# Performance work log

Hardware: AMD Instinct MI355X
Metric: run time of the kernel (lower is better)

## Reference

```python
import jax, jax.numpy as jnp
import numpy as np

N, E = 100000, 1000000
IN_DIM, OUT_DIM, HEADS = 64, 64, 4
C = OUT_DIM // HEADS  # per-head channels = 16
NEG_SLOPE = 0.2
SOFTMAX_EPS = 1e-16  # PyG softmax denominator epsilon
LN_EPS = 1e-5


def setup_inputs() -> dict:
    key = jax.random.key(0)
    ks = jax.random.split(key, 8)
    node_input = jax.random.normal(ks[0], (N, IN_DIM), dtype=jnp.float32)
    edge_index = jax.random.randint(ks[1], (2, E), 0, N, dtype=jnp.int64)
    # GATConv params (glorot-ish scale)
    W = jax.random.normal(ks[2], (IN_DIM, HEADS * C), dtype=jnp.float32) / np.sqrt(IN_DIM)
    att_src = jax.random.normal(ks[3], (HEADS, C), dtype=jnp.float32) / np.sqrt(C)
    att_dst = jax.random.normal(ks[4], (HEADS, C), dtype=jnp.float32) / np.sqrt(C)
    bias = jnp.zeros((HEADS * C,), dtype=jnp.float32)
    # LayerNorm params
    gamma = jnp.ones((OUT_DIM,), dtype=jnp.float32)
    beta = jnp.zeros((OUT_DIM,), dtype=jnp.float32)
    return {"node_input": node_input, "edge_index": edge_index, "W": W,
            "att_src": att_src, "att_dst": att_dst, "bias": bias,
            "gamma": gamma, "beta": beta}


def _gat_forward(x, edge_index, W, att_src, att_dst, bias, gamma, beta):
    src, dst = edge_index[0], edge_index[1]  # message flows src -> dst
    h = (x @ W).reshape(N, HEADS, C)                       # [N, H, C]
    a_src = jnp.einsum('nhc,hc->nh', h, att_src)           # [N, H]
    a_dst = jnp.einsum('nhc,hc->nh', h, att_dst)           # [N, H]
    # per-edge attention logits + leaky relu
    e = a_src[src] + a_dst[dst]                            # [E, H]
    e = jnp.where(e >= 0, e, NEG_SLOPE * e)
    # segment softmax over incoming edges of each target node
    m = jax.ops.segment_max(e, dst, num_segments=N)        # [N, H]
    m = jnp.where(jnp.isfinite(m), m, 0.0)                 # empty segments -> 0
    ex = jnp.exp(e - m[dst])                               # [E, H]
    denom = jax.ops.segment_sum(ex, dst, num_segments=N)   # [N, H]
    alpha = ex / (denom[dst] + SOFTMAX_EPS)                # [E, H]
    # weighted scatter-sum of source features
    msg = alpha[:, :, None] * h[src]                       # [E, H, C]
    out = jax.ops.segment_sum(msg, dst, num_segments=N)    # [N, H, C]
    out = out.reshape(N, HEADS * C) + bias                 # concat heads + bias
    # LayerNorm
    mu = out.mean(axis=-1, keepdims=True)
    var = out.var(axis=-1, keepdims=True)
    out = (out - mu) * jax.lax.rsqrt(var + LN_EPS) * gamma + beta
    # query gate is dead code (graph is a dict -> hasattr fails); dropout is eval identity
    return out


def reference(node_input, edge_index, W, att_src, att_dst, bias, gamma, beta):
    return _gat_forward(node_input, edge_index, W, att_src, att_dst, bias, gamma, beta)
```

## Files before the change

### kernel.cpp

```cpp
#include <hip/hip_runtime.h>
#include <hip/hip_bf16.h>
#include <math.h>

#define N_NODES 100000
#define E_EDGES 1000000
#define HEADS 4
#define DIM 64
#define NEG_SLOPE 0.2f
#define SM_EPS 1e-16f
#define LN_EPS 1e-5f
#define P1_BLOCKS 256
#define NT16 6250
#define GEMM_BLOCKS 1563
#define FEAT_BLOCKS (P1_BLOCKS + GEMM_BLOCKS)
#define CHUNK 3907
#define EPT 16
#define BUCKET_W 512
#define NBUCK 196

typedef __attribute__((ext_vector_type(8))) short short8v;
typedef __attribute__((ext_vector_type(4))) float f32x4;

static __device__ __forceinline__ unsigned short bfh(float f) {
    __hip_bfloat16 b = __float2bfloat16(f);
    return *reinterpret_cast<unsigned short*>(&b);
}
static __device__ __forceinline__ float bfh2f(unsigned short u) {
    return __uint_as_float((unsigned)u << 16);
}

__global__ __launch_bounds__(256) void k_wprep(
        const float* __restrict__ W, uint4* __restrict__ Wf) {
    int t = threadIdx.x;
    for (int e = t; e < 1024; e += 256) {
        int l = e & 63, f = e >> 6;
        int s = f & 1, kh = (f >> 1) & 1, n = f >> 2;
        int c = n * 16 + (l & 15);
        int k0 = kh * 32 + (l >> 4) * 8;
        unsigned short hw[8];
#pragma unroll
        for (int j = 0; j < 8; ++j) {
            float wv = W[(k0 + j) * 64 + c];
            unsigned short hi = bfh(wv);
            hw[j] = s ? bfh(wv - bfh2f(hi)) : hi;
        }
        uint4 pk;
        pk.x = hw[0] | ((unsigned)hw[1] << 16);
        pk.y = hw[2] | ((unsigned)hw[3] << 16);
        pk.z = hw[4] | ((unsigned)hw[5] << 16);
        pk.w = hw[6] | ((unsigned)hw[7] << 16);
        Wf[e] = pk;
    }
}

__global__ __launch_bounds__(256) void k_feat(
        const float* __restrict__ x, const float* __restrict__ Wf_,
        const float* __restrict__ att_src, const float* __restrict__ att_dst,
        const int* __restrict__ ei, __hip_bfloat16* __restrict__ hb,
        float* __restrict__ asrc, float* __restrict__ adst,
        int2* __restrict__ chunkbuf, int* __restrict__ pre) {
    __shared__ __align__(16) int smem_i[8326];
    int t = threadIdx.x;

    if (blockIdx.x < P1_BLOCKS) {
        int2* out2 = (int2*)smem_i;
        int*  cnt  = smem_i + 2 * CHUNK;
        int*  scan = cnt + 256;
        int base_e = blockIdx.x * CHUNK;
        int es[EPT], ed[EPT];
#pragma unroll
        for (int k = 0; k < EPT; ++k) {
            int i = k * 256 + t;
            int e = base_e + i;
            bool v = (i < CHUNK) && (e < E_EDGES);
            es[k] = v ? ei[e] : 0;
            ed[k] = v ? ei[E_EDGES + e] : -1;
        }
        cnt[t] = 0;
        __syncthreads();
#pragma unroll
        for (int k = 0; k < EPT; ++k)
            if (ed[k] >= 0) atomicAdd(&cnt[ed[k] >> 9], 1);
        __syncthreads();
        scan[t] = (t < NBUCK) ? cnt[t] : 0;
        __syncthreads();
#pragma unroll
        for (int off = 1; off < 256; off <<= 1) {
            int v = (t >= off) ? scan[t - off] : 0;
            __syncthreads();
            scan[t] += v;
            __syncthreads();
        }
        int excl = (t == 0) ? 0 : scan[t - 1];
        if (t < NBUCK) pre[blockIdx.x * (NBUCK + 1) + t] = excl;
        if (t == 0)    pre[blockIdx.x * (NBUCK + 1) + NBUCK] = scan[NBUCK - 1];
        if (t < NBUCK) cnt[t] = excl;
        __syncthreads();
#pragma unroll
        for (int k = 0; k < EPT; ++k)
            if (ed[k] >= 0) {
                int pos = atomicAdd(&cnt[ed[k] >> 9], 1);
                out2[pos] = make_int2(es[k], ed[k]);
            }
        __syncthreads();
        int ec = E_EDGES - base_e; ec = (ec > CHUNK) ? CHUNK : ec;
        for (int i = t; i < ec; i += 256)
            chunkbuf[base_e + i] = out2[i];
        return;
    }

    int w = t >> 6, lane = t & 63;
    int tile = (blockIdx.x - P1_BLOCKS) * 4 + w;
    if (tile >= NT16) return;
    int base = tile * 16;
    int m = lane & 15, kg = lane >> 4;

    const float* xr = x + (size_t)(base + m) * 64 + kg * 8;
    short8v ah[2], al[2];
#pragma unroll
    for (int kh = 0; kh < 2; ++kh) {
        float4 q0 = *(const float4*)(xr + kh * 32);
        float4 q1 = *(const float4*)(xr + kh * 32 + 4);
        float qq[8] = {q0.x, q0.y, q0.z, q0.w, q1.x, q1.y, q1.z, q1.w};
#pragma unroll
        for (int j = 0; j < 8; ++j) {
            unsigned short h = bfh(qq[j]);
            ah[kh][j] = (short)h;
            al[kh][j] = (short)bfh(qq[j] - bfh2f(h));
        }
    }

    const short8v* Wfv = (const short8v*)Wf_;
    float vs_keep = 0.f, vd_keep = 0.f;
#pragma unroll
    for (int n = 0; n < 4; ++n) {
        short8v bh0 = Wfv[((n * 2 + 0) * 2 + 0) * 64 + lane];
        short8v bl0 = Wfv[((n * 2 + 0) * 2 + 1) * 64 + lane];
        short8v bh1 = Wfv[((n * 2 + 1) * 2 + 0) * 64 + lane];
        short8v bl1 = Wfv[((n * 2 + 1) * 2 + 1) * 64 + lane];
        f32x4 a4 = {0.f, 0.f, 0.f, 0.f};
        a4 = __builtin_amdgcn_mfma_f32_16x16x32_bf16(ah[0], bh0, a4, 0, 0, 0);
        a4 = __builtin_amdgcn_mfma_f32_16x16x32_bf16(al[0], bh0, a4, 0, 0, 0);
        a4 = __builtin_amdgcn_mfma_f32_16x16x32_bf16(ah[0], bl0, a4, 0, 0, 0);
        a4 = __builtin_amdgcn_mfma_f32_16x16x32_bf16(ah[1], bh1, a4, 0, 0, 0);
        a4 = __builtin_amdgcn_mfma_f32_16x16x32_bf16(al[1], bh1, a4, 0, 0, 0);
        a4 = __builtin_amdgcn_mfma_f32_16x16x32_bf16(ah[1], bl1, a4, 0, 0, 0);
        float asv = att_src[n * 16 + m];
        float adv = att_dst[n * 16 + m];
#pragma unroll
        for (int ri = 0; ri < 4; ++ri) {
            int orow = base + kg * 4 + ri;
            hb[(size_t)orow * 64 + n * 16 + m] = __float2bfloat16(a4[ri]);
            float p = a4[ri] * asv, pd = a4[ri] * adv;
#pragma unroll
            for (int off = 1; off < 16; off <<= 1) {
                p  += __shfl_xor(p,  off, 64);
                pd += __shfl_xor(pd, off, 64);
            }
            if (m == ri * 4 + n) { vs_keep = p; vd_keep = pd; }
        }
    }
    asrc[tile * 64 + kg * 16 + m] = vs_keep;
    adst[tile * 64 + kg * 16 + m] = vd_keep;
}

__global__ __launch_bounds__(256) void k_bin2(
        const int2* __restrict__ chunkbuf, const int* __restrict__ pre,
        int* __restrict__ cursorP, int* __restrict__ srclist) {
    __shared__ int cnt2[BUCKET_W];
    __shared__ int segstart[P1_BLOCKS];
    __shared__ int segpre[P1_BLOCKS + 1];
    __shared__ int scan[P1_BLOCKS];
    int t = threadIdx.x;
    int b = blockIdx.x;
    int nbase = b * BUCKET_W;
    for (int i = t; i < BUCKET_W; i += 256) cnt2[i] = 0;
    int p0 = pre[t * (NBUCK + 1) + b];
    int p1 = pre[t * (NBUCK + 1) + b + 1];
    segstart[t] = t * CHUNK + p0;
    scan[t] = p0;
    __syncthreads();
#pragma unroll
    for (int off = 128; off >= 1; off >>= 1) {
        int v = (t < off) ? scan[t + off] : 0;
        __syncthreads();
        if (t < off) scan[t] += v;
        __syncthreads();
    }
    int gbase = scan[0];
    __syncthreads();
    scan[t] = p1 - p0;
    __syncthreads();
#pragma unroll
    for (int off = 1; off < 256; off <<= 1) {
        int v = (t >= off) ? scan[t - off] : 0;
        __syncthreads();
        scan[t] += v;
        __syncthreads();
    }
    segpre[t + 1] = scan[t];
    if (t == 0) segpre[0] = 0;
    __syncthreads();
    int total = segpre[P1_BLOCKS];
    for (int i = t; i < total; i += 256) {
        int lo = 0, hi = P1_BLOCKS;
#pragma unroll
        for (int it = 0; it < 8; ++it) {
            int mid = (lo + hi) >> 1;
            if (segpre[mid] <= i) lo = mid; else hi = mid;
        }
        int2 e = chunkbuf[segstart[lo] + (i - segpre[lo])];
        atomicAdd(&cnt2[e.y - nbase], 1);
    }
    __syncthreads();
    int c0 = cnt2[2 * t], c1 = cnt2[2 * t + 1];
    scan[t] = c0 + c1;
    __syncthreads();
#pragma unroll
    for (int off = 1; off < 256; off <<= 1) {
        int v = (t >= off) ? scan[t - off] : 0;
        __syncthreads();
        scan[t] += v;
        __syncthreads();
    }
    int pexcl = (t == 0) ? 0 : scan[t - 1];
    cnt2[2 * t]     = pexcl;
    cnt2[2 * t + 1] = pexcl + c0;
    int n0 = nbase + 2 * t;
    if (n0 < N_NODES)     cursorP[n0]     = ((gbase + pexcl) << 6) | c0;
    if (n0 + 1 < N_NODES) cursorP[n0 + 1] = ((gbase + pexcl + c0) << 6) | c1;
    __syncthreads();
    for (int i = t; i < total; i += 256) {
        int lo = 0, hi = P1_BLOCKS;
#pragma unroll
        for (int it = 0; it < 8; ++it) {
            int mid = (lo + hi) >> 1;
            if (segpre[mid] <= i) lo = mid; else hi = mid;
        }
        int2 e = chunkbuf[segstart[lo] + (i - segpre[lo])];
        int pos = atomicAdd(&cnt2[e.y - nbase], 1);
        srclist[gbase + pos] = e.x;
    }
}

__global__ __launch_bounds__(256) void k_aggr(
        const int* __restrict__ cursorP, const int* __restrict__ srclist,
        const float* __restrict__ asrc, const float* __restrict__ adst,
        const __hip_bfloat16* __restrict__ hb,
        const float* __restrict__ bias, const float* __restrict__ gamma,
        const float* __restrict__ beta, float* __restrict__ out) {
    int t = threadIdx.x;
    int lane = t & 63;
    int s = lane >> 5, qq = (lane >> 4) & 1, j = lane & 15;
    int hd = j >> 2;
    int node = blockIdx.x * 8 + (t >> 6) * 2 + s;
    int cw = cursorP[node];
    int dcnt = cw & 63;
    const int* sl = srclist + ((unsigned)cw >> 6);
    int dmax = max(dcnt, __shfl_xor(dcnt, 32, 64));
    const ushort4* hp = (const ushort4*)hb;
    float ad = adst[node * HEADS + hd];
    float acc0 = 0.f, acc1 = 0.f, acc2 = 0.f, acc3 = 0.f, l = 0.f;

    for (int i0 = 0; i0 < dmax; i0 += 8) {
        int idx[4];
        float as[4];
        ushort4 hv[4];
#pragma unroll
        for (int k = 0; k < 4; ++k) {
            int ek = i0 + 2 * k + qq;
            idx[k] = (ek < dcnt) ? sl[ek] : 0;
        }
#pragma unroll
        for (int k = 0; k < 4; ++k) as[k] = asrc[idx[k] * HEADS + hd];
#pragma unroll
        for (int k = 0; k < 4; ++k) hv[k] = hp[idx[k] * 16 + j];
#pragma unroll
        for (int k = 0; k < 4; ++k) {
            int ek = i0 + 2 * k + qq;
            float e = as[k] + ad;
            e = (e >= 0.f) ? e : NEG_SLOPE * e;
            float p = (ek < dcnt) ? __expf(e) : 0.f;
            l += p;
            acc0 += p * __uint_as_float((unsigned)hv[k].x << 16);
            acc1 += p * __uint_as_float((unsigned)hv[k].y << 16);
            acc2 += p * __uint_as_float((unsigned)hv[k].z << 16);
            acc3 += p * __uint_as_float((unsigned)hv[k].w << 16);
        }
    }
    acc0 += __shfl_xor(acc0, 16, 64);
    acc1 += __shfl_xor(acc1, 16, 64);
    acc2 += __shfl_xor(acc2, 16, 64);
    acc3 += __shfl_xor(acc3, 16, 64);
    l    += __shfl_xor(l,    16, 64);

    float inv = 1.f / (l + SM_EPS);
    float4 b4 = ((const float4*)bias)[j];
    float v0 = acc0 * inv + b4.x;
    float v1 = acc1 * inv + b4.y;
    float v2 = acc2 * inv + b4.z;
    float v3 = acc3 * inv + b4.w;
    float s1 = (v0 + v1) + (v2 + v3);
    float s2 = (v0 * v0 + v1 * v1) + (v2 * v2 + v3 * v3);
#pragma unroll
    for (int off = 1; off < 16; off <<= 1) {
        s1 += __shfl_xor(s1, off, 64);
        s2 += __shfl_xor(s2, off, 64);
    }
    float mu = s1 * (1.f / 64.f);
    float var = s2 * (1.f / 64.f) - mu * mu;
    float r = rsqrtf(var + LN_EPS);
    if (qq == 0) {
        float4 g4 = ((const float4*)gamma)[j];
        float4 be4 = ((const float4*)beta)[j];
        float4 o;
        o.x = (v0 - mu) * r * g4.x + be4.x;
        o.y = (v1 - mu) * r * g4.y + be4.y;
        o.z = (v2 - mu) * r * g4.z + be4.z;
        o.w = (v3 - mu) * r * g4.w + be4.w;
        ((float4*)(out + (size_t)node * DIM))[j] = o;
    }
}

extern "C" void kernel_launch(void* const* d_in, const int* in_sizes, int n_in,
                              void* d_out, int out_size, void* d_ws, size_t ws_size,
                              hipStream_t stream) {
    const float* x       = (const float*)d_in[0];
    const int*   ei      = (const int*)d_in[1];
    const float* W       = (const float*)d_in[2];
    const float* att_src = (const float*)d_in[3];
    const float* att_dst = (const float*)d_in[4];
    const float* bias    = (const float*)d_in[5];
    const float* gamma   = (const float*)d_in[6];
    const float* beta    = (const float*)d_in[7];
    float* out = (float*)d_out;

    int2* chunkbuf = (int2*)d_ws;
    int*  pre      = (int*)(chunkbuf + (size_t)P1_BLOCKS * CHUNK);
    int*  cursorP  = pre + (size_t)P1_BLOCKS * (NBUCK + 1);
    int*  srclist  = cursorP + N_NODES;
    float* asrc    = (float*)(srclist + (size_t)E_EDGES);
    float* adst    = asrc + (size_t)N_NODES * HEADS;
    __hip_bfloat16* hb = (__hip_bfloat16*)(adst + (size_t)N_NODES * HEADS);
    uint4* Wf      = (uint4*)(hb + (size_t)N_NODES * DIM);

    k_wprep<<<1, 256, 0, stream>>>(W, Wf);
    k_feat<<<FEAT_BLOCKS, 256, 0, stream>>>(x, (const float*)Wf, att_src,
                                            att_dst, ei, hb, asrc, adst,
                                            chunkbuf, pre);
    k_bin2<<<NBUCK, 256, 0, stream>>>(chunkbuf, pre, cursorP, srclist);
    k_aggr<<<N_NODES / 8, 256, 0, stream>>>(cursorP, srclist, asrc, adst, hb,
                                            bias, gamma, beta, out);
}
```

Baseline: 166.9 us.

## Split binning from GEMM, widen bin kernels to 1024 threads, cache edges

Splits the fused feature kernel into a separate edge-binning kernel and a GEMM kernel, so they no longer share one launch. Both binning passes now use 1024-thread blocks, spreading each chunk's or bucket's edges over more threads. The second binning pass keeps the edges it loaded in registers, so the scatter pass reuses them instead of redoing the binary search and global reload. In exchange it adds one more launch and drops the old overlap of binning with GEMM inside one grid, and the larger blocks use more registers.

```diff
diff --git a/kernel.cpp b/kernel.cpp
--- a/kernel.cpp
+++ b/kernel.cpp
@@ -12,11 +12,10 @@
 #define P1_BLOCKS 256
 #define NT16 6250
 #define GEMM_BLOCKS 1563
-#define FEAT_BLOCKS (P1_BLOCKS + GEMM_BLOCKS)
 #define CHUNK 3907
-#define EPT 16
 #define BUCKET_W 512
 #define NBUCK 196
+#define MAXE2 8
 
 typedef __attribute__((ext_vector_type(8))) short short8v;
 typedef __attribute__((ext_vector_type(4))) float f32x4;
@@ -53,64 +52,65 @@
     }
 }
 
-__global__ __launch_bounds__(256) void k_feat(
-        const float* __restrict__ x, const float* __restrict__ Wf_,
-        const float* __restrict__ att_src, const float* __restrict__ att_dst,
-        const int* __restrict__ ei, __hip_bfloat16* __restrict__ hb,
-        float* __restrict__ asrc, float* __restrict__ adst,
+__global__ __launch_bounds__(1024) void k_bin(
+        const int* __restrict__ ei,
         int2* __restrict__ chunkbuf, int* __restrict__ pre) {
-    __shared__ __align__(16) int smem_i[8326];
-    int t = threadIdx.x;
-
-    if (blockIdx.x < P1_BLOCKS) {
-        int2* out2 = (int2*)smem_i;
-        int*  cnt  = smem_i + 2 * CHUNK;
-        int*  scan = cnt + 256;
-        int base_e = blockIdx.x * CHUNK;
-        int es[EPT], ed[EPT];
-#pragma unroll
-        for (int k = 0; k < EPT; ++k) {
-            int i = k * 256 + t;
-            int e = base_e + i;
-            bool v = (i < CHUNK) && (e < E_EDGES);
-            es[k] = v ? ei[e] : 0;
-            ed[k] = v ? ei[E_EDGES + e] : -1;
-        }
-        cnt[t] = 0;
-        __syncthreads();
-#pragma unroll
-        for (int k = 0; k < EPT; ++k)
-            if (ed[k] >= 0) atomicAdd(&cnt[ed[k] >> 9], 1);
-        __syncthreads();
-        scan[t] = (t < NBUCK) ? cnt[t] : 0;
-        __syncthreads();
-#pragma unroll
-        for (int off = 1; off < 256; off <<= 1) {
-            int v = (t >= off) ? scan[t - off] : 0;
-            __syncthreads();
-            scan[t] += v;
-            __syncthreads();
-        }
+    __shared__ __align__(16) int2 out2[CHUNK];
+    __shared__ int cnt[256];
+    __shared__ int scan[256];
+    int t = threadIdx.x;
+    int base_e = blockIdx.x * CHUNK;
+    int es[4], ed[4];
+#pragma unroll
+    for (int k = 0; k < 4; ++k) {
+        int i = k * 1024 + t;
+        int e = base_e + i;
+        bool v = (i < CHUNK) && (e < E_EDGES);
+        es[k] = v ? ei[e] : 0;
+        ed[k] = v ? ei[E_EDGES + e] : -1;
+    }
+    if (t < 256) cnt[t] = 0;
+    __syncthreads();
+#pragma unroll
+    for (int k = 0; k < 4; ++k)
+        if (ed[k] >= 0) atomicAdd(&cnt[ed[k] >> 9], 1);
+    __syncthreads();
+    if (t < 256) scan[t] = (t < NBUCK) ? cnt[t] : 0;
+    __syncthreads();
+#pragma unroll
+    for (int off = 1; off < 256; off <<= 1) {
+        int v = (t >= off && t < 256) ? scan[t - off] : 0;
+        __syncthreads();
+        if (t < 256) scan[t] += v;
+        __syncthreads();
+    }
+    if (t < 256) {
         int excl = (t == 0) ? 0 : scan[t - 1];
         if (t < NBUCK) pre[blockIdx.x * (NBUCK + 1) + t] = excl;
         if (t == 0)    pre[blockIdx.x * (NBUCK + 1) + NBUCK] = scan[NBUCK - 1];
         if (t < NBUCK) cnt[t] = excl;
-        __syncthreads();
-#pragma unroll
-        for (int k = 0; k < EPT; ++k)
-            if (ed[k] >= 0) {
-                int pos = atomicAdd(&cnt[ed[k] >> 9], 1);
-                out2[pos] = make_int2(es[k], ed[k]);
-            }
-        __syncthreads();
-        int ec = E_EDGES - base_e; ec = (ec > CHUNK) ? CHUNK : ec;
-        for (int i = t; i < ec; i += 256)
-            chunkbuf[base_e + i] = out2[i];
-        return;
-    }
-
+    }
+    __syncthreads();
+#pragma unroll
+    for (int k = 0; k < 4; ++k)
+        if (ed[k] >= 0) {
+            int pos = atomicAdd(&cnt[ed[k] >> 9], 1);
+            out2[pos] = make_int2(es[k], ed[k]);
+        }
+    __syncthreads();
+    int ec = E_EDGES - base_e; ec = (ec > CHUNK) ? CHUNK : ec;
+    for (int i = t; i < ec; i += 1024)
+        chunkbuf[base_e + i] = out2[i];
+}
+
+__global__ __launch_bounds__(256) void k_gemm(
+        const float* __restrict__ x, const float* __restrict__ Wf_,
+        const float* __restrict__ att_src, const float* __restrict__ att_dst,
+        __hip_bfloat16* __restrict__ hb,
+        float* __restrict__ asrc, float* __restrict__ adst) {
+    int t = threadIdx.x;
     int w = t >> 6, lane = t & 63;
-    int tile = (blockIdx.x - P1_BLOCKS) * 4 + w;
+    int tile = blockIdx.x * 4 + w;
     if (tile >= NT16) return;
     int base = tile * 16;
     int m = lane & 15, kg = lane >> 4;
@@ -164,7 +164,7 @@
     adst[tile * 64 + kg * 16 + m] = vd_keep;
 }
 
-__global__ __launch_bounds__(256) void k_bin2(
+__global__ __launch_bounds__(1024) void k_bin2(
         const int2* __restrict__ chunkbuf, const int* __restrict__ pre,
         int* __restrict__ cursorP, int* __restrict__ srclist) {
     __shared__ int cnt2[BUCKET_W];
@@ -174,11 +174,14 @@
     int t = threadIdx.x;
     int b = blockIdx.x;
     int nbase = b * BUCKET_W;
-    for (int i = t; i < BUCKET_W; i += 256) cnt2[i] = 0;
-    int p0 = pre[t * (NBUCK + 1) + b];
-    int p1 = pre[t * (NBUCK + 1) + b + 1];
-    segstart[t] = t * CHUNK + p0;
-    scan[t] = p0;
+    if (t < BUCKET_W) cnt2[t] = 0;
+    int p0 = 0, p1 = 0;
+    if (t < 256) {
+        p0 = pre[t * (NBUCK + 1) + b];
+        p1 = pre[t * (NBUCK + 1) + b + 1];
+        segstart[t] = t * CHUNK + p0;
+        scan[t] = p0;
+    }
     __syncthreads();
 #pragma unroll
     for (int off = 128; off >= 1; off >>= 1) {
@@ -189,20 +192,36 @@
     }
     int gbase = scan[0];
     __syncthreads();
-    scan[t] = p1 - p0;
+    if (t < 256) scan[t] = p1 - p0;
     __syncthreads();
 #pragma unroll
     for (int off = 1; off < 256; off <<= 1) {
-        int v = (t >= off) ? scan[t - off] : 0;
-        __syncthreads();
-        scan[t] += v;
-        __syncthreads();
-    }
-    segpre[t + 1] = scan[t];
+        int v = (t >= off && t < 256) ? scan[t - off] : 0;
+        __syncthreads();
+        if (t < 256) scan[t] += v;
+        __syncthreads();
+    }
+    if (t < 256) segpre[t + 1] = scan[t];
     if (t == 0) segpre[0] = 0;
     __syncthreads();
     int total = segpre[P1_BLOCKS];
-    for (int i = t; i < total; i += 256) {
+    int2 ecache[MAXE2];
+#pragma unroll
+    for (int ii = 0; ii < MAXE2; ++ii) {
+        int i = ii * 1024 + t;
+        if (i < total) {
+            int lo = 0, hi = P1_BLOCKS;
+#pragma unroll
+            for (int it = 0; it < 8; ++it) {
+                int mid = (lo + hi) >> 1;
+                if (segpre[mid] <= i) lo = mid; else hi = mid;
+            }
+            int2 e = chunkbuf[segstart[lo] + (i - segpre[lo])];
+            ecache[ii] = e;
+            atomicAdd(&cnt2[e.y - nbase], 1);
+        }
+    }
+    for (int i = MAXE2 * 1024 + t; i < total; i += 1024) {
         int lo = 0, hi = P1_BLOCKS;
 #pragma unroll
         for (int it = 0; it < 8; ++it) {
@@ -213,24 +232,38 @@
         atomicAdd(&cnt2[e.y - nbase], 1);
     }
     __syncthreads();
-    int c0 = cnt2[2 * t], c1 = cnt2[2 * t + 1];
-    scan[t] = c0 + c1;
+    int c0 = 0, c1 = 0;
+    if (t < 256) {
+        c0 = cnt2[2 * t]; c1 = cnt2[2 * t + 1];
+        scan[t] = c0 + c1;
+    }
     __syncthreads();
 #pragma unroll
     for (int off = 1; off < 256; off <<= 1) {
-        int v = (t >= off) ? scan[t - off] : 0;
-        __syncthreads();
-        scan[t] += v;
-        __syncthreads();
-    }
-    int pexcl = (t == 0) ? 0 : scan[t - 1];
-    cnt2[2 * t]     = pexcl;
-    cnt2[2 * t + 1] = pexcl + c0;
-    int n0 = nbase + 2 * t;
-    if (n0 < N_NODES)     cursorP[n0]     = ((gbase + pexcl) << 6) | c0;
-    if (n0 + 1 < N_NODES) cursorP[n0 + 1] = ((gbase + pexcl + c0) << 6) | c1;
-    __syncthreads();
-    for (int i = t; i < total; i += 256) {
+        int v = (t >= off && t < 256) ? scan[t - off] : 0;
+        __syncthreads();
+        if (t < 256) scan[t] += v;
+        __syncthreads();
+    }
+    if (t < 256) {
+        int pexcl = (t == 0) ? 0 : scan[t - 1];
+        cnt2[2 * t]     = pexcl;
+        cnt2[2 * t + 1] = pexcl + c0;
+        int n0 = nbase + 2 * t;
+        if (n0 < N_NODES)     cursorP[n0]     = ((gbase + pexcl) << 6) | c0;
+        if (n0 + 1 < N_NODES) cursorP[n0 + 1] = ((gbase + pexcl + c0) << 6) | c1;
+    }
+    __syncthreads();
+#pragma unroll
+    for (int ii = 0; ii < MAXE2; ++ii) {
+        int i = ii * 1024 + t;
+        if (i < total) {
+            int2 e = ecache[ii];
+            int pos = atomicAdd(&cnt2[e.y - nbase], 1);
+            srclist[gbase + pos] = e.x;
+        }
+    }
+    for (int i = MAXE2 * 1024 + t; i < total; i += 1024) {
         int lo = 0, hi = P1_BLOCKS;
 #pragma unroll
         for (int it = 0; it < 8; ++it) {
@@ -345,10 +378,10 @@
     uint4* Wf      = (uint4*)(hb + (size_t)N_NODES * DIM);
 
     k_wprep<<<1, 256, 0, stream>>>(W, Wf);
-    k_feat<<<FEAT_BLOCKS, 256, 0, stream>>>(x, (const float*)Wf, att_src,
-                                            att_dst, ei, hb, asrc, adst,
-                                            chunkbuf, pre);
-    k_bin2<<<NBUCK, 256, 0, stream>>>(chunkbuf, pre, cursorP, srclist);
+    k_bin<<<P1_BLOCKS, 1024, 0, stream>>>(ei, chunkbuf, pre);
+    k_gemm<<<GEMM_BLOCKS, 256, 0, stream>>>(x, (const float*)Wf, att_src,
+                                            att_dst, hb, asrc, adst);
+    k_bin2<<<NBUCK, 1024, 0, stream>>>(chunkbuf, pre, cursorP, srclist);
     k_aggr<<<N_NODES / 8, 256, 0, stream>>>(cursorP, srclist, asrc, adst, hb,
                                             bias, gamma, beta, out);
 }
```

New measurement: 156.1 us. -6.4%, faster.
